# Kernel optimization log

Hardware: AMD Instinct MI355X
Metric: run time of the kernel (lower is better)

The kernel has to match this reference:

```python
import jax, jax.numpy as jnp
import numpy as np

N, D, R, NREL, E = 100000, 128, 8, 16, 250000
ADAPTER_SCALE = 1.0


def _xavier(key, shape, fan_in, fan_out):
    lim = float(np.sqrt(6.0 / (fan_in + fan_out)))
    return jax.random.uniform(key, shape, jnp.float32, -lim, lim)


def setup_inputs() -> dict:
    key = jax.random.key(0)
    ks = jax.random.split(key, 12)
    x = jax.random.normal(ks[0], (N, D), jnp.float32)
    edge_index = jax.random.randint(ks[1], (2, E), 0, N, jnp.int64)
    edge_type = jax.random.randint(ks[2], (E,), 0, NREL, jnp.int64)
    # parameters
    W = _xavier(ks[3], (D, D), D, D)                      # W.weight [out,in]
    eps = jnp.zeros((1,), jnp.float32)
    A_emb = _xavier(ks[4], (NREL, D * R), NREL, D * R)
    B_emb = _xavier(ks[5], (NREL, D * R), NREL, D * R)
    # MLP: d -> 2d -> 2d -> d (biases default True in nn.Linear)
    W1 = _xavier(ks[6], (2 * D, D), D, 2 * D)
    b1 = jnp.zeros((2 * D,), jnp.float32)
    W2 = _xavier(ks[7], (2 * D, 2 * D), 2 * D, 2 * D)
    b2 = jnp.zeros((2 * D,), jnp.float32)
    W3 = _xavier(ks[8], (D, 2 * D), 2 * D, D)
    b3 = jnp.zeros((D,), jnp.float32)
    return {"x": x, "edge_index": edge_index, "edge_type": edge_type,
            "W": W, "eps": eps, "A_emb": A_emb, "B_emb": B_emb,
            "W1": W1, "b1": b1, "W2": W2, "b2": b2, "W3": W3, "b3": b3}


def reference(x, edge_index, edge_type, W, eps, A_emb, B_emb, W1, b1, W2, b2, W3, b3):
    src, dst = edge_index[0], edge_index[1]
    x_j = x[src]                                  # [E, d] gather
    base = x_j @ W.T                              # [E, d]
    A = A_emb[edge_type].reshape(-1, D, R)        # [E, d, r]
    B = B_emb[edge_type].reshape(-1, D, R)        # [E, d, r]
    Bj = jnp.einsum('edk,ed->ek', B, x_j)         # [E, r]
    adapter = jnp.einsum('edk,ek->ed', A, Bj)     # [E, d]
    msg = base + ADAPTER_SCALE * adapter
    aggr = jax.ops.segment_sum(msg, dst, num_segments=N)  # scatter-add
    out = (1.0 + eps) * x + aggr                  # GIN update
    h = jax.nn.relu(out @ W1.T + b1)
    h = jax.nn.relu(h @ W2.T + b2)
    return h @ W3.T + b3
```

## Files before the change

kernel.cpp:

```cpp
#include <hip/hip_runtime.h>
#include <stdint.h>

#define N_NODES 100000
#define DIM     128
#define RANK    8
#define N_REL   16
#define N_EDGE  250000

#define SCAN_BLOCKS 391
#define NSTRIPS     6250

typedef __attribute__((ext_vector_type(8))) short  short8v;
typedef __attribute__((ext_vector_type(4))) float  float4v;

__device__ inline unsigned short f2bf(float f) {
    union { float f; unsigned u; } v; v.f = f;
    unsigned r = v.u + 0x7fffu + ((v.u >> 16) & 1u);
    return (unsigned short)(r >> 16);
}
__device__ inline float bf2f(unsigned short h) {
    union { unsigned u; float f; } v; v.u = ((unsigned)h) << 16;
    return v.f;
}

__global__ __launch_bounds__(256) void wcvt_kernel(
    const float* __restrict__ W,  const float* __restrict__ W1,
    const float* __restrict__ W2, const float* __restrict__ W3,
    const float* __restrict__ Ae, const float* __restrict__ Be,
    unsigned short* __restrict__ out)
{
    int i = blockIdx.x * blockDim.x + threadIdx.x;
    if (i >= 180224) return;
    float v;
    if      (i <  16384) v = W[i];
    else if (i <  32768) {
        int j = i - 16384; int c = j >> 7, d = j & 127;
        v = Be[(c >> 3) * 1024 + d * 8 + (c & 7)];
    }
    else if (i <  65536) v = W1[i - 32768];
    else if (i < 131072) v = W2[i - 65536];
    else if (i < 163840) v = W3[i - 131072];
    else                 v = Ae[i - 163840];
    out[i] = f2bf(v);
}

__global__ __launch_bounds__(256) void hist_kernel(
    const int* __restrict__ eidx, int* __restrict__ deg)
{
    int e = blockIdx.x * 256 + threadIdx.x;
    if (e < N_EDGE) atomicAdd(&deg[eidx[N_EDGE + e]], 1);
}

__global__ __launch_bounds__(256) void scan_part_kernel(
    const int* __restrict__ deg, int* __restrict__ bsum)
{
    const int idx  = blockIdx.x * 256 + threadIdx.x;
    const int lane = threadIdx.x & 63, wid = threadIdx.x >> 6;
    __shared__ int ws[4];
    int v = (idx < N_NODES) ? deg[idx] : 0;
    #pragma unroll
    for (int off = 1; off < 64; off <<= 1) v += __shfl_xor(v, off);
    if (lane == 0) ws[wid] = v;
    __syncthreads();
    if (threadIdx.x == 0) bsum[blockIdx.x] = ws[0] + ws[1] + ws[2] + ws[3];
}

__global__ __launch_bounds__(512) void scan_bsum_kernel(
    const int* __restrict__ bsum, int* __restrict__ bpre)
{
    const int t = threadIdx.x;
    const int lane = t & 63, wid = t >> 6;
    __shared__ int ws[8];
    int v = (t < SCAN_BLOCKS) ? bsum[t] : 0;
    int inc = v;
    #pragma unroll
    for (int off = 1; off < 64; off <<= 1) {
        int u = __shfl_up(inc, off);
        if (lane >= off) inc += u;
    }
    if (lane == 63) ws[wid] = inc;
    __syncthreads();
    if (wid == 0) {
        int u = (lane < 8) ? ws[lane] : 0;
        int winc = u;
        #pragma unroll
        for (int off = 1; off < 8; off <<= 1) {
            int w = __shfl_up(winc, off);
            if (lane >= off) winc += w;
        }
        if (lane < 8) ws[lane] = winc - u;
    }
    __syncthreads();
    if (t < SCAN_BLOCKS) bpre[t] = ws[wid] + (inc - v);
}

__global__ __launch_bounds__(256) void scan_final_kernel(
    const int* __restrict__ deg, const int* __restrict__ bpre,
    int* __restrict__ offsets, int* __restrict__ wo)
{
    const int idx  = blockIdx.x * 256 + threadIdx.x;
    const int lane = threadIdx.x & 63, wid = threadIdx.x >> 6;
    __shared__ int ws[4];
    int v = (idx < N_NODES) ? deg[idx] : 0;
    int inc = v;
    #pragma unroll
    for (int off = 1; off < 64; off <<= 1) {
        int u = __shfl_up(inc, off);
        if (lane >= off) inc += u;
    }
    if (lane == 63) ws[wid] = inc;
    __syncthreads();
    int wbase = 0;
    #pragma unroll
    for (int w = 0; w < 4; ++w) wbase += (w < wid) ? ws[w] : 0;
    if (idx < N_NODES) {
        int ex = bpre[blockIdx.x] + wbase + (inc - v);
        offsets[idx] = ex;
        wo[idx]      = ex;
    }
    if (blockIdx.x == 0 && threadIdx.x == 0) offsets[N_NODES] = N_EDGE;
}

__global__ __launch_bounds__(256) void scatter_kernel(
    const int* __restrict__ eidx, const int* __restrict__ etype,
    int* __restrict__ wo, int* __restrict__ sorted)
{
    int e = blockIdx.x * 256 + threadIdx.x;
    if (e < N_EDGE) {
        int pos = atomicAdd(&wo[eidx[N_EDGE + e]], 1);
        sorted[pos] = eidx[e] | (etype[e] << 20);
    }
}

__global__ __launch_bounds__(256) void aggr_kernel(
    const float*          __restrict__ x,
    const unsigned short* __restrict__ ybj,
    const unsigned short* __restrict__ Ab,
    const int*            __restrict__ offsets,
    const int*            __restrict__ sorted,
    const float*          __restrict__ epsp,
    unsigned short*       __restrict__ h0)
{
    const int lane = threadIdx.x & 63;
    const int node = blockIdx.x * 4 + (threadIdx.x >> 6);
    if (node >= N_NODES) return;

    const int beg = offsets[node], end = offsets[node + 1];
    float acc0 = 0.f, acc1 = 0.f;

    for (int i = beg; i < end; ++i) {
        const unsigned p = (unsigned)sorted[i];
        const int src = p & 0xFFFFF;
        const int rt  = p >> 20;

        short8v bj = *reinterpret_cast<const short8v*>(
            ybj + (size_t)src * 256 + 128 + rt * 8);
        const unsigned short* ap = Ab + rt * 1024 + 16 * lane;
        short8v a0 = *reinterpret_cast<const short8v*>(ap);
        short8v a1 = *reinterpret_cast<const short8v*>(ap + 8);
        unsigned yv = *reinterpret_cast<const unsigned*>(
            ybj + (size_t)src * 256 + 2 * lane);

        float ad0 = 0.f, ad1 = 0.f;
        #pragma unroll
        for (int k = 0; k < 8; ++k) {
            float pv = bf2f((unsigned short)bj[k]);
            ad0 += bf2f((unsigned short)a0[k]) * pv;
            ad1 += bf2f((unsigned short)a1[k]) * pv;
        }
        acc0 += bf2f((unsigned short)(yv & 0xffffu)) + ad0;
        acc1 += bf2f((unsigned short)(yv >> 16)) + ad1;
    }

    const float s1 = 1.0f + epsp[0];
    float2 xv = *reinterpret_cast<const float2*>(x + (size_t)node * DIM + 2 * lane);
    unsigned o = (unsigned)f2bf(s1 * xv.x + acc0)
               | ((unsigned)f2bf(s1 * xv.y + acc1) << 16);
    *reinterpret_cast<unsigned*>(h0 + (size_t)node * DIM + 2 * lane) = o;
}

template<int K, int NOUT, int AMODE, int OMODE>
__global__ __launch_bounds__(512) void wsgemm(
    const void*           __restrict__ Aptr,
    const unsigned short* __restrict__ Wb,
    const float*          __restrict__ bias,
    void*                 __restrict__ Out)
{
    constexpr int KT = K / 32;
    constexpr int NSLICE = NOUT / 32;
    constexpr int SGRP = 8 / NSLICE;

    const int lane  = threadIdx.x & 63;
    const int w     = threadIdx.x >> 6;
    const int slice = w % NSLICE;
    const int sgrp  = w / NSLICE;
    const int row16 = lane & 15;
    const int kgrp  = lane >> 4;

    short8v bfrag[2][KT];
    #pragma unroll
    for (int nt = 0; nt < 2; ++nt) {
        const int n = slice * 32 + nt * 16 + row16;
        #pragma unroll
        for (int kt = 0; kt < KT; ++kt)
            bfrag[nt][kt] = *reinterpret_cast<const short8v*>(
                Wb + (size_t)n * K + kt * 32 + kgrp * 8);
    }

    float bv0 = 0.f, bv1 = 0.f;
    if constexpr (OMODE != 0) {
        bv0 = bias[slice * 32 + row16];
        bv1 = bias[slice * 32 + 16 + row16];
    }

    for (int strip = blockIdx.x * SGRP + sgrp; strip < NSTRIPS;
         strip += gridDim.x * SGRP)
    {
        const int m = strip * 16 + row16;
        short8v afrag[KT];
        #pragma unroll
        for (int kt = 0; kt < KT; ++kt) {
            const int k0 = kt * 32 + kgrp * 8;
            if constexpr (AMODE == 2) {
                afrag[kt] = *reinterpret_cast<const short8v*>(
                    (const unsigned short*)Aptr + (size_t)m * K + k0);
            } else {
                const float* ap = (const float*)Aptr + (size_t)m * K + k0;
                float4v v0 = *reinterpret_cast<const float4v*>(ap);
                float4v v1 = *reinterpret_cast<const float4v*>(ap + 4);
                short8v f;
                #pragma unroll
                for (int j = 0; j < 4; ++j) {
                    f[j]     = (short)f2bf(v0[j]);
                    f[4 + j] = (short)f2bf(v1[j]);
                }
                afrag[kt] = f;
            }
        }

        float4v acc0 = {0.f, 0.f, 0.f, 0.f};
        float4v acc1 = {0.f, 0.f, 0.f, 0.f};
        #pragma unroll
        for (int kt = 0; kt < KT; ++kt) {
            acc0 = __builtin_amdgcn_mfma_f32_16x16x32_bf16(
                afrag[kt], bfrag[0][kt], acc0, 0, 0, 0);
            acc1 = __builtin_amdgcn_mfma_f32_16x16x32_bf16(
                afrag[kt], bfrag[1][kt], acc1, 0, 0, 0);
        }

        #pragma unroll
        for (int r = 0; r < 4; ++r) {
            const int mr = strip * 16 + kgrp * 4 + r;
            float v0 = acc0[r], v1 = acc1[r];
            if constexpr (OMODE == 1) {
                v0 = fmaxf(v0 + bv0, 0.f);
                v1 = fmaxf(v1 + bv1, 0.f);
            }
            if constexpr (OMODE == 2) { v0 += bv0; v1 += bv1; }
            if constexpr (OMODE == 2) {
                ((float*)Out)[(size_t)mr * NOUT + slice * 32 + row16]      = v0;
                ((float*)Out)[(size_t)mr * NOUT + slice * 32 + 16 + row16] = v1;
            } else {
                ((unsigned short*)Out)[(size_t)mr * NOUT + slice * 32 + row16]      = f2bf(v0);
                ((unsigned short*)Out)[(size_t)mr * NOUT + slice * 32 + 16 + row16] = f2bf(v1);
            }
        }
    }
}

__global__ __launch_bounds__(512, 2) void mlp_fused(
    const unsigned short* __restrict__ h0,
    const unsigned short* __restrict__ W1b,
    const float*          __restrict__ b1,
    const unsigned short* __restrict__ W2b,
    const float*          __restrict__ b2,
    const unsigned short* __restrict__ W3b,
    const float*          __restrict__ b3,
    float*                __restrict__ out)
{
    __shared__ unsigned short lbuf[2][2][16 * 256];

    const int lane  = threadIdx.x & 63;
    const int w     = threadIdx.x >> 6;
    const int row16 = lane & 15;
    const int kgrp  = lane >> 4;

    short8v w1f[2][4], w2f[2][8], w3f[8];
    #pragma unroll
    for (int nt = 0; nt < 2; ++nt) {
        const int n = w * 32 + nt * 16 + row16;
        #pragma unroll
        for (int kt = 0; kt < 4; ++kt)
            w1f[nt][kt] = *reinterpret_cast<const short8v*>(
                W1b + (size_t)n * 128 + kt * 32 + kgrp * 8);
        #pragma unroll
        for (int kt = 0; kt < 8; ++kt)
            w2f[nt][kt] = *reinterpret_cast<const short8v*>(
                W2b + (size_t)n * 256 + kt * 32 + kgrp * 8);
    }
    {
        const int n = w * 16 + row16;
        #pragma unroll
        for (int kt = 0; kt < 8; ++kt)
            w3f[kt] = *reinterpret_cast<const short8v*>(
                W3b + (size_t)n * 256 + kt * 32 + kgrp * 8);
    }
    const float bv1[2] = {b1[w*32 + row16], b1[w*32 + 16 + row16]};
    const float bv2[2] = {b2[w*32 + row16], b2[w*32 + 16 + row16]};
    const float bv3    = b3[w*16 + row16];

    int p = 0;
    for (int strip = blockIdx.x; strip < NSTRIPS; strip += gridDim.x, p ^= 1) {
        short8v af[8];
        #pragma unroll
        for (int kt = 0; kt < 4; ++kt)
            af[kt] = *reinterpret_cast<const short8v*>(
                h0 + (size_t)(strip * 16 + row16) * 128 + kt * 32 + kgrp * 8);

        float4v acc0 = {0.f,0.f,0.f,0.f}, acc1 = {0.f,0.f,0.f,0.f};
        #pragma unroll
        for (int kt = 0; kt < 4; ++kt) {
            acc0 = __builtin_amdgcn_mfma_f32_16x16x32_bf16(af[kt], w1f[0][kt], acc0, 0,0,0);
            acc1 = __builtin_amdgcn_mfma_f32_16x16x32_bf16(af[kt], w1f[1][kt], acc1, 0,0,0);
        }
        char* const l1 = (char*)&lbuf[p][0][0];
        #pragma unroll
        for (int nt = 0; nt < 2; ++nt) {
            #pragma unroll
            for (int r = 0; r < 4; ++r) {
                const int rw = kgrp * 4 + r;
                const int cb = (w * 32 + nt * 16 + row16) * 2;
                const float v = fmaxf((nt ? acc1[r] : acc0[r]) + bv1[nt], 0.f);
                *(unsigned short*)(l1 + rw * 512 + (cb ^ ((rw & 7) << 4))) = f2bf(v);
            }
        }
        __syncthreads();

        #pragma unroll
        for (int kt = 0; kt < 8; ++kt)
            af[kt] = *reinterpret_cast<const short8v*>(
                l1 + row16 * 512 + ((kt * 64 + kgrp * 16) ^ ((row16 & 7) << 4)));

        acc0 = (float4v){0.f,0.f,0.f,0.f}; acc1 = (float4v){0.f,0.f,0.f,0.f};
        #pragma unroll
        for (int kt = 0; kt < 8; ++kt) {
            acc0 = __builtin_amdgcn_mfma_f32_16x16x32_bf16(af[kt], w2f[0][kt], acc0, 0,0,0);
            acc1 = __builtin_amdgcn_mfma_f32_16x16x32_bf16(af[kt], w2f[1][kt], acc1, 0,0,0);
        }
        char* const l2 = (char*)&lbuf[p][1][0];
        #pragma unroll
        for (int nt = 0; nt < 2; ++nt) {
            #pragma unroll
            for (int r = 0; r < 4; ++r) {
                const int rw = kgrp * 4 + r;
                const int cb = (w * 32 + nt * 16 + row16) * 2;
                const float v = fmaxf((nt ? acc1[r] : acc0[r]) + bv2[nt], 0.f);
                *(unsigned short*)(l2 + rw * 512 + (cb ^ ((rw & 7) << 4))) = f2bf(v);
            }
        }
        __syncthreads();

        #pragma unroll
        for (int kt = 0; kt < 8; ++kt)
            af[kt] = *reinterpret_cast<const short8v*>(
                l2 + row16 * 512 + ((kt * 64 + kgrp * 16) ^ ((row16 & 7) << 4)));

        float4v a3 = {0.f,0.f,0.f,0.f};
        #pragma unroll
        for (int kt = 0; kt < 8; ++kt)
            a3 = __builtin_amdgcn_mfma_f32_16x16x32_bf16(af[kt], w3f[kt], a3, 0,0,0);

        #pragma unroll
        for (int r = 0; r < 4; ++r)
            out[(size_t)(strip * 16 + kgrp * 4 + r) * 128 + w * 16 + row16] = a3[r] + bv3;
    }
}

extern "C" void kernel_launch(void* const* d_in, const int* in_sizes, int n_in,
                              void* d_out, int out_size, void* d_ws, size_t ws_size,
                              hipStream_t stream)
{
    const float* x     = (const float*)d_in[0];
    const int*   eidx  = (const int*)  d_in[1];
    const int*   etype = (const int*)  d_in[2];
    const float* W     = (const float*)d_in[3];
    const float* eps   = (const float*)d_in[4];
    const float* A_emb = (const float*)d_in[5];
    const float* B_emb = (const float*)d_in[6];
    const float* W1    = (const float*)d_in[7];
    const float* b1    = (const float*)d_in[8];
    const float* W2    = (const float*)d_in[9];
    const float* b2    = (const float*)d_in[10];
    const float* W3    = (const float*)d_in[11];
    const float* b3    = (const float*)d_in[12];

    char* wsb = (char*)d_ws;
    unsigned short* ybj  = (unsigned short*)(wsb);
    unsigned short* h0   = (unsigned short*)(wsb + 51200000);
    int*            deg     = (int*)(wsb + 76800000);
    int*            offsets = (int*)(wsb + 76800000 + 400000);
    int*            wo      = (int*)(wsb + 76800000 + 800004);
    int*            sorted  = (int*)(wsb + 76800000 + 1200004);
    int*            bsum    = (int*)(wsb + 76800000 + 2200008);
    int*            bpre    = (int*)(wsb + 76800000 + 2201576);
    unsigned short* wts  = (unsigned short*)(wsb + 102400000);

    unsigned short* WyB = wts;
    unsigned short* W1b = wts + 32768;
    unsigned short* W2b = wts + 65536;
    unsigned short* W3b = wts + 131072;
    unsigned short* Ab  = wts + 163840;

    wcvt_kernel<<<704, 256, 0, stream>>>(W, W1, W2, W3, A_emb, B_emb, wts);

    hipMemsetAsync(deg, 0, N_NODES * sizeof(int), stream);

    wsgemm<128, 256, 0, 0><<<1024, 512, 0, stream>>>(x, WyB, nullptr, ybj);

    hist_kernel      <<<977, 256, 0, stream>>>(eidx, deg);
    scan_part_kernel <<<SCAN_BLOCKS, 256, 0, stream>>>(deg, bsum);
    scan_bsum_kernel <<<1, 512, 0, stream>>>(bsum, bpre);
    scan_final_kernel<<<SCAN_BLOCKS, 256, 0, stream>>>(deg, bpre, offsets, wo);
    scatter_kernel   <<<977, 256, 0, stream>>>(eidx, etype, wo, sorted);

    aggr_kernel<<<25000, 256, 0, stream>>>(x, ybj, Ab, offsets, sorted, eps, h0);

    mlp_fused<<<1024, 512, 0, stream>>>(h0, W1b, b1, W2b, b2, W3b, b3, (float*)d_out);
}
```

Before: 330.6 us.

## Retile ybj GEMM and MLP to 32-row strips, prefetch edge index in aggregation

The x·[W;B] projection becomes a dedicated 256-thread kernel in which each wave computes 64 output columns of a 16-row strip. Each x row is now loaded and converted to bf16 once instead of once per column slice. The fused MLP processes 32 rows per iteration with single LDS buffers and a wider swizzle, which halves the grid and the number of barriers per row. Empty asm constraints pin the weight fragments in registers. The aggregation loop software-prefetches the next sorted edge entry. Together these raise register pressure and lower occupancy, and dropping double buffering may add stalls at the LDS barriers.

New measurement: 301.1 us. 8.9% less time.

```diff
diff --git a/kernel.cpp b/kernel.cpp
--- a/kernel.cpp
+++ b/kernel.cpp
@@ -9,6 +9,7 @@
 
 #define SCAN_BLOCKS 391
 #define NSTRIPS     6250
+#define NSTRIPS32   3125
 
 typedef __attribute__((ext_vector_type(8))) short  short8v;
 typedef __attribute__((ext_vector_type(4))) float  float4v;
@@ -148,28 +149,33 @@
     const int beg = offsets[node], end = offsets[node + 1];
     float acc0 = 0.f, acc1 = 0.f;
 
-    for (int i = beg; i < end; ++i) {
-        const unsigned p = (unsigned)sorted[i];
-        const int src = p & 0xFFFFF;
-        const int rt  = p >> 20;
-
-        short8v bj = *reinterpret_cast<const short8v*>(
-            ybj + (size_t)src * 256 + 128 + rt * 8);
-        const unsigned short* ap = Ab + rt * 1024 + 16 * lane;
-        short8v a0 = *reinterpret_cast<const short8v*>(ap);
-        short8v a1 = *reinterpret_cast<const short8v*>(ap + 8);
-        unsigned yv = *reinterpret_cast<const unsigned*>(
-            ybj + (size_t)src * 256 + 2 * lane);
-
-        float ad0 = 0.f, ad1 = 0.f;
-        #pragma unroll
-        for (int k = 0; k < 8; ++k) {
-            float pv = bf2f((unsigned short)bj[k]);
-            ad0 += bf2f((unsigned short)a0[k]) * pv;
-            ad1 += bf2f((unsigned short)a1[k]) * pv;
-        }
-        acc0 += bf2f((unsigned short)(yv & 0xffffu)) + ad0;
-        acc1 += bf2f((unsigned short)(yv >> 16)) + ad1;
+    if (beg < end) {
+        unsigned p = (unsigned)sorted[beg];
+        for (int i = beg; i < end; ++i) {
+            const int src = p & 0xFFFFF;
+            const int rt  = p >> 20;
+
+            short8v bj = *reinterpret_cast<const short8v*>(
+                ybj + (size_t)src * 256 + 128 + rt * 8);
+            const unsigned short* ap = Ab + rt * 1024 + 16 * lane;
+            short8v a0 = *reinterpret_cast<const short8v*>(ap);
+            short8v a1 = *reinterpret_cast<const short8v*>(ap + 8);
+            unsigned yv = *reinterpret_cast<const unsigned*>(
+                ybj + (size_t)src * 256 + 2 * lane);
+
+            const int inext = (i + 1 < end) ? (i + 1) : i;
+            p = (unsigned)sorted[inext];
+
+            float ad0 = 0.f, ad1 = 0.f;
+            #pragma unroll
+            for (int k = 0; k < 8; ++k) {
+                float pv = bf2f((unsigned short)bj[k]);
+                ad0 += bf2f((unsigned short)a0[k]) * pv;
+                ad1 += bf2f((unsigned short)a1[k]) * pv;
+            }
+            acc0 += bf2f((unsigned short)(yv & 0xffffu)) + ad0;
+            acc1 += bf2f((unsigned short)(yv >> 16)) + ad1;
+        }
     }
 
     const float s1 = 1.0f + epsp[0];
@@ -179,91 +185,63 @@
     *reinterpret_cast<unsigned*>(h0 + (size_t)node * DIM + 2 * lane) = o;
 }
 
-template<int K, int NOUT, int AMODE, int OMODE>
-__global__ __launch_bounds__(512) void wsgemm(
-    const void*           __restrict__ Aptr,
+__global__ __launch_bounds__(256) void ybj_gemm(
+    const float*          __restrict__ x,
     const unsigned short* __restrict__ Wb,
-    const float*          __restrict__ bias,
-    void*                 __restrict__ Out)
-{
-    constexpr int KT = K / 32;
-    constexpr int NSLICE = NOUT / 32;
-    constexpr int SGRP = 8 / NSLICE;
-
+    unsigned short*       __restrict__ Out)
+{
     const int lane  = threadIdx.x & 63;
     const int w     = threadIdx.x >> 6;
-    const int slice = w % NSLICE;
-    const int sgrp  = w / NSLICE;
     const int row16 = lane & 15;
     const int kgrp  = lane >> 4;
 
-    short8v bfrag[2][KT];
-    #pragma unroll
-    for (int nt = 0; nt < 2; ++nt) {
-        const int n = slice * 32 + nt * 16 + row16;
-        #pragma unroll
-        for (int kt = 0; kt < KT; ++kt)
+    short8v bfrag[4][4];
+    #pragma unroll
+    for (int nt = 0; nt < 4; ++nt) {
+        const int n = w * 64 + nt * 16 + row16;
+        #pragma unroll
+        for (int kt = 0; kt < 4; ++kt)
             bfrag[nt][kt] = *reinterpret_cast<const short8v*>(
-                Wb + (size_t)n * K + kt * 32 + kgrp * 8);
-    }
-
-    float bv0 = 0.f, bv1 = 0.f;
-    if constexpr (OMODE != 0) {
-        bv0 = bias[slice * 32 + row16];
-        bv1 = bias[slice * 32 + 16 + row16];
-    }
-
-    for (int strip = blockIdx.x * SGRP + sgrp; strip < NSTRIPS;
-         strip += gridDim.x * SGRP)
-    {
-        const int m = strip * 16 + row16;
-        short8v afrag[KT];
-        #pragma unroll
-        for (int kt = 0; kt < KT; ++kt) {
-            const int k0 = kt * 32 + kgrp * 8;
-            if constexpr (AMODE == 2) {
-                afrag[kt] = *reinterpret_cast<const short8v*>(
-                    (const unsigned short*)Aptr + (size_t)m * K + k0);
-            } else {
-                const float* ap = (const float*)Aptr + (size_t)m * K + k0;
-                float4v v0 = *reinterpret_cast<const float4v*>(ap);
-                float4v v1 = *reinterpret_cast<const float4v*>(ap + 4);
-                short8v f;
-                #pragma unroll
-                for (int j = 0; j < 4; ++j) {
-                    f[j]     = (short)f2bf(v0[j]);
-                    f[4 + j] = (short)f2bf(v1[j]);
-                }
-                afrag[kt] = f;
+                Wb + (size_t)n * 128 + kt * 32 + kgrp * 8);
+    }
+
+    for (int s = blockIdx.x; s < NSTRIPS; s += gridDim.x) {
+        const float* ap = x + (size_t)(s * 16 + row16) * 128;
+        float4v v[8];
+        #pragma unroll
+        for (int kt = 0; kt < 4; ++kt) {
+            v[2*kt]   = *reinterpret_cast<const float4v*>(ap + kt * 32 + kgrp * 8);
+            v[2*kt+1] = *reinterpret_cast<const float4v*>(ap + kt * 32 + kgrp * 8 + 4);
+        }
+        short8v af[4];
+        #pragma unroll
+        for (int kt = 0; kt < 4; ++kt) {
+            short8v f;
+            #pragma unroll
+            for (int j = 0; j < 4; ++j) {
+                f[j]     = (short)f2bf(v[2*kt][j]);
+                f[4 + j] = (short)f2bf(v[2*kt+1][j]);
             }
-        }
-
-        float4v acc0 = {0.f, 0.f, 0.f, 0.f};
-        float4v acc1 = {0.f, 0.f, 0.f, 0.f};
-        #pragma unroll
-        for (int kt = 0; kt < KT; ++kt) {
-            acc0 = __builtin_amdgcn_mfma_f32_16x16x32_bf16(
-                afrag[kt], bfrag[0][kt], acc0, 0, 0, 0);
-            acc1 = __builtin_amdgcn_mfma_f32_16x16x32_bf16(
-                afrag[kt], bfrag[1][kt], acc1, 0, 0, 0);
-        }
-
-        #pragma unroll
-        for (int r = 0; r < 4; ++r) {
-            const int mr = strip * 16 + kgrp * 4 + r;
-            float v0 = acc0[r], v1 = acc1[r];
-            if constexpr (OMODE == 1) {
-                v0 = fmaxf(v0 + bv0, 0.f);
-                v1 = fmaxf(v1 + bv1, 0.f);
-            }
-            if constexpr (OMODE == 2) { v0 += bv0; v1 += bv1; }
-            if constexpr (OMODE == 2) {
-                ((float*)Out)[(size_t)mr * NOUT + slice * 32 + row16]      = v0;
-                ((float*)Out)[(size_t)mr * NOUT + slice * 32 + 16 + row16] = v1;
-            } else {
-                ((unsigned short*)Out)[(size_t)mr * NOUT + slice * 32 + row16]      = f2bf(v0);
-                ((unsigned short*)Out)[(size_t)mr * NOUT + slice * 32 + 16 + row16] = f2bf(v1);
-            }
+            af[kt] = f;
+        }
+
+        float4v acc[4];
+        #pragma unroll
+        for (int nt = 0; nt < 4; ++nt) acc[nt] = (float4v){0.f,0.f,0.f,0.f};
+        #pragma unroll
+        for (int kt = 0; kt < 4; ++kt) {
+            #pragma unroll
+            for (int nt = 0; nt < 4; ++nt)
+                acc[nt] = __builtin_amdgcn_mfma_f32_16x16x32_bf16(
+                    af[kt], bfrag[nt][kt], acc[nt], 0, 0, 0);
+        }
+
+        #pragma unroll
+        for (int nt = 0; nt < 4; ++nt) {
+            #pragma unroll
+            for (int r = 0; r < 4; ++r)
+                Out[(size_t)(s * 16 + kgrp * 4 + r) * 256 + w * 64 + nt * 16 + row16]
+                    = f2bf(acc[nt][r]);
         }
     }
 }
@@ -278,7 +256,8 @@
     const float*          __restrict__ b3,
     float*                __restrict__ out)
 {
-    __shared__ unsigned short lbuf[2][2][16 * 256];
+    __shared__ unsigned short l1s[32 * 256];
+    __shared__ unsigned short l2s[32 * 256];
 
     const int lane  = threadIdx.x & 63;
     const int w     = threadIdx.x >> 6;
@@ -305,74 +284,102 @@
             w3f[kt] = *reinterpret_cast<const short8v*>(
                 W3b + (size_t)n * 256 + kt * 32 + kgrp * 8);
     }
+    #pragma unroll
+    for (int nt = 0; nt < 2; ++nt) {
+        #pragma unroll
+        for (int kt = 0; kt < 4; ++kt) asm volatile("" : "+v"(w1f[nt][kt]));
+        #pragma unroll
+        for (int kt = 0; kt < 8; ++kt) asm volatile("" : "+v"(w2f[nt][kt]));
+    }
+    #pragma unroll
+    for (int kt = 0; kt < 8; ++kt) asm volatile("" : "+v"(w3f[kt]));
+
     const float bv1[2] = {b1[w*32 + row16], b1[w*32 + 16 + row16]};
     const float bv2[2] = {b2[w*32 + row16], b2[w*32 + 16 + row16]};
     const float bv3    = b3[w*16 + row16];
 
-    int p = 0;
-    for (int strip = blockIdx.x; strip < NSTRIPS; strip += gridDim.x, p ^= 1) {
+    char* const l1 = (char*)l1s;
+    char* const l2 = (char*)l2s;
+
+    for (int strip = blockIdx.x; strip < NSTRIPS32; strip += gridDim.x) {
         short8v af[8];
         #pragma unroll
-        for (int kt = 0; kt < 4; ++kt)
-            af[kt] = *reinterpret_cast<const short8v*>(
-                h0 + (size_t)(strip * 16 + row16) * 128 + kt * 32 + kgrp * 8);
-
-        float4v acc0 = {0.f,0.f,0.f,0.f}, acc1 = {0.f,0.f,0.f,0.f};
-        #pragma unroll
-        for (int kt = 0; kt < 4; ++kt) {
-            acc0 = __builtin_amdgcn_mfma_f32_16x16x32_bf16(af[kt], w1f[0][kt], acc0, 0,0,0);
-            acc1 = __builtin_amdgcn_mfma_f32_16x16x32_bf16(af[kt], w1f[1][kt], acc1, 0,0,0);
-        }
-        char* const l1 = (char*)&lbuf[p][0][0];
-        #pragma unroll
-        for (int nt = 0; nt < 2; ++nt) {
-            #pragma unroll
-            for (int r = 0; r < 4; ++r) {
-                const int rw = kgrp * 4 + r;
-                const int cb = (w * 32 + nt * 16 + row16) * 2;
-                const float v = fmaxf((nt ? acc1[r] : acc0[r]) + bv1[nt], 0.f);
-                *(unsigned short*)(l1 + rw * 512 + (cb ^ ((rw & 7) << 4))) = f2bf(v);
+        for (int t = 0; t < 2; ++t)
+            #pragma unroll
+            for (int kt = 0; kt < 4; ++kt)
+                af[t*4 + kt] = *reinterpret_cast<const short8v*>(
+                    h0 + (size_t)(strip * 32 + t * 16 + row16) * 128 + kt * 32 + kgrp * 8);
+
+        float4v a1acc[2][2];
+        #pragma unroll
+        for (int t = 0; t < 2; ++t)
+            #pragma unroll
+            for (int nt = 0; nt < 2; ++nt) a1acc[t][nt] = (float4v){0.f,0.f,0.f,0.f};
+        #pragma unroll
+        for (int t = 0; t < 2; ++t)
+            #pragma unroll
+            for (int kt = 0; kt < 4; ++kt) {
+                a1acc[t][0] = __builtin_amdgcn_mfma_f32_16x16x32_bf16(af[t*4+kt], w1f[0][kt], a1acc[t][0], 0,0,0);
+                a1acc[t][1] = __builtin_amdgcn_mfma_f32_16x16x32_bf16(af[t*4+kt], w1f[1][kt], a1acc[t][1], 0,0,0);
             }
-        }
+        #pragma unroll
+        for (int t = 0; t < 2; ++t)
+            #pragma unroll
+            for (int nt = 0; nt < 2; ++nt)
+                #pragma unroll
+                for (int r = 0; r < 4; ++r) {
+                    const int rw = t * 16 + kgrp * 4 + r;
+                    const int cb = (w * 32 + nt * 16 + row16) * 2;
+                    const float v = fmaxf(a1acc[t][nt][r] + bv1[nt], 0.f);
+                    *(unsigned short*)(l1 + rw * 512 + (cb ^ ((rw & 15) << 4))) = f2bf(v);
+                }
         __syncthreads();
 
-        #pragma unroll
-        for (int kt = 0; kt < 8; ++kt)
-            af[kt] = *reinterpret_cast<const short8v*>(
-                l1 + row16 * 512 + ((kt * 64 + kgrp * 16) ^ ((row16 & 7) << 4)));
-
-        acc0 = (float4v){0.f,0.f,0.f,0.f}; acc1 = (float4v){0.f,0.f,0.f,0.f};
-        #pragma unroll
-        for (int kt = 0; kt < 8; ++kt) {
-            acc0 = __builtin_amdgcn_mfma_f32_16x16x32_bf16(af[kt], w2f[0][kt], acc0, 0,0,0);
-            acc1 = __builtin_amdgcn_mfma_f32_16x16x32_bf16(af[kt], w2f[1][kt], acc1, 0,0,0);
-        }
-        char* const l2 = (char*)&lbuf[p][1][0];
-        #pragma unroll
-        for (int nt = 0; nt < 2; ++nt) {
-            #pragma unroll
-            for (int r = 0; r < 4; ++r) {
-                const int rw = kgrp * 4 + r;
-                const int cb = (w * 32 + nt * 16 + row16) * 2;
-                const float v = fmaxf((nt ? acc1[r] : acc0[r]) + bv2[nt], 0.f);
-                *(unsigned short*)(l2 + rw * 512 + (cb ^ ((rw & 7) << 4))) = f2bf(v);
+        float4v a2acc[2][2];
+        #pragma unroll
+        for (int t = 0; t < 2; ++t) {
+            const int rloc = t * 16 + row16;
+            #pragma unroll
+            for (int kt = 0; kt < 8; ++kt)
+                af[kt] = *reinterpret_cast<const short8v*>(
+                    l1 + rloc * 512 + ((kt * 64 + kgrp * 16) ^ ((rloc & 15) << 4)));
+            a2acc[t][0] = (float4v){0.f,0.f,0.f,0.f};
+            a2acc[t][1] = (float4v){0.f,0.f,0.f,0.f};
+            #pragma unroll
+            for (int kt = 0; kt < 8; ++kt) {
+                a2acc[t][0] = __builtin_amdgcn_mfma_f32_16x16x32_bf16(af[kt], w2f[0][kt], a2acc[t][0], 0,0,0);
+                a2acc[t][1] = __builtin_amdgcn_mfma_f32_16x16x32_bf16(af[kt], w2f[1][kt], a2acc[t][1], 0,0,0);
             }
         }
+        #pragma unroll
+        for (int t = 0; t < 2; ++t)
+            #pragma unroll
+            for (int nt = 0; nt < 2; ++nt)
+                #pragma unroll
+                for (int r = 0; r < 4; ++r) {
+                    const int rw = t * 16 + kgrp * 4 + r;
+                    const int cb = (w * 32 + nt * 16 + row16) * 2;
+                    const float v = fmaxf(a2acc[t][nt][r] + bv2[nt], 0.f);
+                    *(unsigned short*)(l2 + rw * 512 + (cb ^ ((rw & 15) << 4))) = f2bf(v);
+                }
         __syncthreads();
 
         #pragma unroll
-        for (int kt = 0; kt < 8; ++kt)
-            af[kt] = *reinterpret_cast<const short8v*>(
-                l2 + row16 * 512 + ((kt * 64 + kgrp * 16) ^ ((row16 & 7) << 4)));
-
-        float4v a3 = {0.f,0.f,0.f,0.f};
-        #pragma unroll
-        for (int kt = 0; kt < 8; ++kt)
-            a3 = __builtin_amdgcn_mfma_f32_16x16x32_bf16(af[kt], w3f[kt], a3, 0,0,0);
-
-        #pragma unroll
-        for (int r = 0; r < 4; ++r)
-            out[(size_t)(strip * 16 + kgrp * 4 + r) * 128 + w * 16 + row16] = a3[r] + bv3;
+        for (int t = 0; t < 2; ++t) {
+            const int rloc = t * 16 + row16;
+            #pragma unroll
+            for (int kt = 0; kt < 8; ++kt)
+                af[kt] = *reinterpret_cast<const short8v*>(
+                    l2 + rloc * 512 + ((kt * 64 + kgrp * 16) ^ ((rloc & 15) << 4)));
+            float4v a3 = {0.f,0.f,0.f,0.f};
+            #pragma unroll
+            for (int kt = 0; kt < 8; ++kt)
+                a3 = __builtin_amdgcn_mfma_f32_16x16x32_bf16(af[kt], w3f[kt], a3, 0,0,0);
+            #pragma unroll
+            for (int r = 0; r < 4; ++r)
+                out[(size_t)(strip * 32 + t * 16 + kgrp * 4 + r) * 128 + w * 16 + row16]
+                    = a3[r] + bv3;
+        }
     }
 }
 
@@ -415,7 +422,7 @@
 
     hipMemsetAsync(deg, 0, N_NODES * sizeof(int), stream);
 
-    wsgemm<128, 256, 0, 0><<<1024, 512, 0, stream>>>(x, WyB, nullptr, ybj);
+    ybj_gemm<<<1024, 256, 0, stream>>>(x, WyB, ybj);
 
     hist_kernel      <<<977, 256, 0, stream>>>(eidx, deg);
     scan_part_kernel <<<SCAN_BLOCKS, 256, 0, stream>>>(deg, bsum);
@@ -425,5 +432,5 @@
 
     aggr_kernel<<<25000, 256, 0, stream>>>(x, ybj, Ab, offsets, sorted, eps, h0);
 
-    mlp_fused<<<1024, 512, 0, stream>>>(h0, W1b, b1, W2b, b2, W3b, b3, (float*)d_out);
-}
+    mlp_fused<<<512, 512, 0, stream>>>(h0, W1b, b1, W2b, b2, W3b, b3, (float*)d_out);
+}
```
